# Performance work log

Hardware: AMD Instinct MI355X
Metric: run time of the kernel (lower is better)

Reference implementation:

```python
import jax, jax.numpy as jnp
import numpy as np
from jax import lax

EPS = 1e-5

def _ln(x, g, b):
    m = x.mean(-1, keepdims=True)
    v = x.var(-1, keepdims=True)
    return (x - m) * lax.rsqrt(v + EPS) * g + b

def _conv(x, w, b=None, groups=1, pad=0):
    y = lax.conv_general_dilated(x, w, (1, 1), [(pad, pad), (pad, pad)],
                                 feature_group_count=groups,
                                 dimension_numbers=('NCHW', 'OIHW', 'NCHW'))
    return y if b is None else y + b[None, :, None, None]

def _pscan(A, X):
    # linear recurrence h_t = A_t * h_{t-1} + X_t via associative scan over axis 1
    def comb(c1, c2):
        a1, x1 = c1
        a2, x2 = c2
        return a1 * a2, a2 * x1 + x2
    return lax.associative_scan(comb, (A, X), axis=1)[1]

def setup_inputs():
    B, T, D, H, W, K, E = 2, 24, 32, 64, 64, 3, 2
    key = jax.random.key(0)
    ks = jax.random.split(key, 30)
    r = lambda i, shp, s=1.0: jax.random.normal(ks[i], shp, jnp.float32) * s
    return dict(
        x_re=r(0, (B, T, D, H, W)), x_im=r(1, (B, T, D, H, W)),
        h_re=r(2, (B * H * W, 1, D)), h_im=r(3, (B * H * W, 1, D)),
        flux_re=r(4, (B, D), 0.5), flux_im=r(5, (B, D), 0.5),
        dt_seq=jax.random.uniform(ks[6], (B, T), jnp.float32, 0.05, 0.15),
        ln_s_g=jnp.ones((2 * D,)), ln_s_b=jnp.zeros((2 * D,)),
        conv_w=r(7, (2 * D, 2 * D, K, K), 0.05), conv_b=jnp.zeros((2 * D,)),
        ln_t_g=jnp.ones((2 * D,)), ln_t_b=jnp.zeros((2 * D,)),
        W_re=jnp.eye(D, dtype=jnp.float32) + r(8, (D, D), 0.1), W_im=r(9, (D, D), 0.1),
        lam_flux=r(10, (D,), 0.5), bf_re=r(11, (D,), 0.5), bf_im=r(12, (D,), 0.5),
        c_re=r(13, (D,), 0.5), c_im=r(14, (D,), 0.5),
        g_w=r(15, (D,), 0.5), g_b=jnp.zeros((D,)),
        a_decay=r(16, (D,), 0.5), b_freq=r(17, (D,), 0.5),
        ffn_w1=r(18, (2 * D, 2 * D * E), 0.05), ffn_b1=jnp.zeros((2 * D * E,)),
        ffn_w2=r(19, (2 * D * E, 2 * D), 0.05), ffn_b2=jnp.zeros((2 * D,)),
        sg_w1=r(20, (D, 2 * D, 1, 1), 0.05), sg_b1=jnp.zeros((D,)),
        sg_dw=r(21, (D, 1, 3, 3), 0.05),
        sg_w2=r(22, (D, D, 1, 1), 0.05), sg_b2=jnp.zeros((D,)),
    )

def reference(x_re, x_im, h_re, h_im, flux_re, flux_im, dt_seq,
              ln_s_g, ln_s_b, conv_w, conv_b, ln_t_g, ln_t_b,
              W_re, W_im, lam_flux, bf_re, bf_im, c_re, c_im, g_w, g_b,
              a_decay, b_freq, ffn_w1, ffn_b1, ffn_w2, ffn_b2,
              sg_w1, sg_b1, sg_dw, sg_w2, sg_b2):
    x = x_re + 1j * x_im                                  # [B,T,D,H,W] complex64
    B, T, D, H, W = x.shape
    K = conv_w.shape[-1]
    # ---- spatial (Clifford-style) conv with residual ----
    xf = x.reshape(B * T, D, H, W)
    xr = jnp.concatenate([xf.real, xf.imag], axis=1)      # [BT,2D,H,W]
    xn = _ln(xr.transpose(0, 2, 3, 1), ln_s_g, ln_s_b).transpose(0, 3, 1, 2)
    xs = _conv(xn, conv_w, conv_b, pad=K // 2)
    xf = xf + (xs[:, :D] + 1j * xs[:, D:])
    x = xf.reshape(B, T, D, H, W)
    # ---- eigen-basis encode ----
    Wb = W_re + 1j * W_im
    Wb_inv = jnp.linalg.inv(Wb)
    x_eig = jnp.einsum('bthwd,de->bthwe', x.transpose(0, 1, 3, 4, 2), Wb)  # [B,T,H,W,D]
    x_mean = x_eig.mean(axis=(2, 3))                      # [B,T,D]
    # ---- global flux scan over time ----
    dt = dt_seq[:, :, None]                               # [B,T,1]
    A_flux = jnp.exp(-jax.nn.softplus(lam_flux) * dt).astype(x_eig.dtype)  # [B,T,D]
    X_flux = (bf_re + 1j * bf_im) * x_mean * dt
    flux_seq = _pscan(A_flux, X_flux)
    flux_seq = flux_seq + (flux_re + 1j * flux_im)[:, None, :] * jnp.cumprod(A_flux, axis=1)
    source_seq = flux_seq * (c_re + 1j * c_im)            # [B,T,D] complex
    gate_seq = jax.nn.sigmoid(flux_seq.real * g_w + g_b)  # [B,T,D] real
    flux_out = flux_seq[:, -1]
    # ---- spatial gate modulation, batched over B*T (no python loop over T) ----
    xc = jnp.concatenate([x_eig.real, x_eig.imag], axis=-1)        # [B,T,H,W,2D]
    sf = xc.reshape(B * T, H, W, 2 * D).transpose(0, 3, 1, 2)
    g = jax.nn.silu(_conv(sf, sg_w1, sg_b1))
    g = _conv(g, sg_dw, None, groups=D, pad=1)
    g = jax.nn.sigmoid(_conv(g, sg_w2, sg_b2))                     # [BT,D,H,W]
    sp_gate = g.transpose(0, 2, 3, 1).reshape(B, T, H, W, D)
    gate_comb = gate_seq[:, :, None, None, :] * sp_gate            # [B,T,H,W,D]
    src = source_seq[:, :, None, None, :]
    forcing = x_eig * gate_comb + src * (1.0 - gate_comb)
    # ---- transition operators (ZOH discretization) ----
    lam = -jax.nn.softplus(a_decay) + 1j * b_freq                  # [D]
    op_decay = jnp.exp(lam * dt)                                   # [B,T,D] complex
    op_forcing = (op_decay - 1.0) / lam
    u_t = forcing * op_forcing[:, :, None, None, :]
    h_prev = (h_re + 1j * h_im).reshape(B, H, W, D)
    u_t = u_t.at[:, 0].add(h_prev * op_decay[:, 0][:, None, None, :])
    # ---- per-pixel temporal pscan ----
    A_full = jnp.broadcast_to(op_decay[:, :, None, None, :], u_t.shape)
    u_out = _pscan(A_full, u_t)                                    # [B,T,H,W,D]
    h_out = u_out[:, -1].reshape(B * H * W, 1, D)
    # ---- decode + temporal LN/FFN residual ----
    dec = jnp.einsum('bthwe,ed->bthwd', u_out, Wb_inv).transpose(0, 1, 4, 2, 3)
    df = dec.reshape(B * T, D, H, W)
    dr = jnp.concatenate([df.real, df.imag], axis=1).transpose(0, 2, 3, 1)  # [BT,H,W,2D]
    dn = _ln(dr, ln_t_g, ln_t_b)
    hid = jax.nn.silu(dn @ ffn_w1 + ffn_b1)
    out2 = hid @ ffn_w2 + ffn_b2
    delta = (out2[..., :D] + 1j * out2[..., D:]).transpose(0, 3, 1, 2)
    xo = (df + delta).reshape(B, T, D, H, W)
    z = x + xo
    out_main = jnp.stack([z.real, z.imag], axis=0)
    out_h = jnp.stack([h_out.real, h_out.imag], axis=0)
    out_flux = jnp.stack([flux_out.real, flux_out.imag], axis=0)
    return out_main, out_h, out_flux
```

## Files before the change

kernel.cpp:

```cpp
#include <hip/hip_runtime.h>
#include <math.h>

#define BB 2
#define TT 24
#define DD 32
#define HWp 4096
#define NN (BB*TT)
#define PIX (NN*HWp)
#define C2 (2*DD)

#define MAIN_RE 0
#define MAIN_IM (NN*DD*HWp)
#define HOUT_RE (2*NN*DD*HWp)
#define HOUT_IM (HOUT_RE + BB*HWp*DD)
#define FLUX_RE (HOUT_RE + 2*BB*HWp*DD)
#define FLUX_IM (FLUX_RE + BB*DD)

#define WS_XN   0
#define WS_XU   (WS_XN + PIX*32)
#define WS_XE   (WS_XU + PIX*32)
#define WS_G1   (WS_XE + PIX*C2)
#define WS_G2   (WS_G1 + PIX*DD)
#define WS_WINV (WS_G2 + PIX*DD)
#define WS_SUMS (WS_WINV + 2048)
#define WS_GATE (WS_SUMS + 3072)
#define WS_SRCR (WS_GATE + 1536)
#define WS_SRCI (WS_SRCR + 1536)
#define WS_ODR  (WS_SRCI + 1536)
#define WS_ODI  (WS_ODR + 1536)
#define WS_OFR  (WS_ODI + 1536)
#define WS_OFI  (WS_OFR + 1536)
#define WS_WPK  (WS_OFI + 1536)
#define WS_PART (WS_WPK + 18432)
#define WS_WE   (WS_PART + 49152)
#define WS_SG   (WS_WE + 2048)
#define WS_WIB  (WS_SG + 1024)

typedef __attribute__((ext_vector_type(8))) short bf16x8;
typedef __attribute__((ext_vector_type(4))) float f32x4;
union FU { unsigned u[4]; bf16x8 f; };
union FU4 { uint4 v; unsigned u[4]; bf16x8 f; };

__device__ __forceinline__ float sigmoidf_(float x) { return 1.f / (1.f + expf(-x)); }
__device__ __forceinline__ float softplusf_(float x) { return log1pf(expf(x)); }
__device__ __forceinline__ unsigned short f2bf(float f) {
  unsigned u = __float_as_uint(f);
  return (unsigned short)((u + 0x7FFFu + ((u >> 16) & 1u)) >> 16);
}
__device__ __forceinline__ unsigned pk2(float lo, float hi) {
  return (unsigned)f2bf(lo) | ((unsigned)f2bf(hi) << 16);
}
__device__ __forceinline__ float bf2f(unsigned short u) {
  return __uint_as_float((unsigned)u << 16);
}

__global__ void __launch_bounds__(256) k_prep(
    const float* __restrict__ xre, const float* __restrict__ xim,
    const float* __restrict__ g, const float* __restrict__ b,
    const float* __restrict__ Wre, const float* __restrict__ Wim,
    const float* __restrict__ conv_w, const float* __restrict__ sgw1,
    float* __restrict__ ws) {
  __shared__ float Mre[32][64];
  __shared__ float Mim[32][64];
  __shared__ float fre[32], fim[32];
  __shared__ int piv_s;
  int bid = blockIdx.x;
  int tid = threadIdx.x;

  if (bid < 768) {
    int gid = bid * 256 + tid;
    int n = gid >> 12, p = gid & 4095;
    float v[64];
    float s = 0.f;
#pragma unroll
    for (int c = 0; c < 32; ++c) { v[c] = xre[(n * 32 + c) * 4096 + p]; s += v[c]; }
#pragma unroll
    for (int c = 0; c < 32; ++c) { v[32 + c] = xim[(n * 32 + c) * 4096 + p]; s += v[32 + c]; }
    float m = s * (1.f / 64.f);
    float vs = 0.f;
#pragma unroll
    for (int c = 0; c < 64; ++c) { float d = v[c] - m; vs += d * d; }
    float rs = rsqrtf(vs * (1.f / 64.f) + 1e-5f);
#pragma unroll
    for (int c = 0; c < 64; ++c) v[c] = (v[c] - m) * rs * g[c] + b[c];
    uint4* dst = (uint4*)ws + gid * 8;
#pragma unroll
    for (int q = 0; q < 8; ++q) {
      uint4 u;
      u.x = pk2(v[q * 8 + 0], v[q * 8 + 1]);
      u.y = pk2(v[q * 8 + 2], v[q * 8 + 3]);
      u.z = pk2(v[q * 8 + 4], v[q * 8 + 5]);
      u.w = pk2(v[q * 8 + 6], v[q * 8 + 7]);
      dst[q] = u;
    }
    return;
  }

  if (bid == 768) {
    for (int idx = tid; idx < 2048; idx += 256) {
      int i = idx >> 6, j = idx & 63;
      if (j < 32) { Mre[i][j] = Wre[i * 32 + j]; Mim[i][j] = Wim[i * 32 + j]; }
      else        { Mre[i][j] = (j - 32 == i) ? 1.f : 0.f; Mim[i][j] = 0.f; }
    }
    __syncthreads();
    for (int k = 0; k < 32; ++k) {
      if (tid < 64) {
        int r = tid & 31;
        float mm = (r >= k) ? (fabsf(Mre[r][k]) + fabsf(Mim[r][k])) : -1.f;
        int best = r;
#pragma unroll
        for (int off = 16; off > 0; off >>= 1) {
          float m2 = __shfl_xor(mm, off);
          int b2 = __shfl_xor(best, off);
          if (m2 > mm || (m2 == mm && b2 < best)) { mm = m2; best = b2; }
        }
        if (tid == 0) piv_s = best;
      }
      __syncthreads();
      int pv = piv_s;
      if (pv != k && tid < 64) {
        float tr = Mre[k][tid], ti = Mim[k][tid];
        Mre[k][tid] = Mre[pv][tid]; Mim[k][tid] = Mim[pv][tid];
        Mre[pv][tid] = tr; Mim[pv][tid] = ti;
      }
      __syncthreads();
      float a = Mre[k][k], bq = Mim[k][k];
      float dd = a * a + bq * bq;
      float pr = a / dd, pi = -bq / dd;
      if (tid < 64) {
        float x = Mre[k][tid], y = Mim[k][tid];
        Mre[k][tid] = x * pr - y * pi;
        Mim[k][tid] = x * pi + y * pr;
      }
      __syncthreads();
      if (tid < 32) { fre[tid] = Mre[tid][k]; fim[tid] = Mim[tid][k]; }
      __syncthreads();
      for (int idx = tid; idx < 2048; idx += 256) {
        int i = idx >> 6, j = idx & 63;
        if (i != k) {
          float fr = fre[i], fi = fim[i];
          float ar = Mre[k][j], ai = Mim[k][j];
          Mre[i][j] -= fr * ar - fi * ai;
          Mim[i][j] -= fr * ai + fi * ar;
        }
      }
      __syncthreads();
    }
    unsigned* wib = (unsigned*)(ws + WS_WIB);
    for (int idx = tid; idx < 2048; idx += 256) {
      int j = idx >> 5, kp = idx & 31;
      float v[2];
#pragma unroll
      for (int h = 0; h < 2; ++h) {
        int k = 2 * kp + h;
        float x;
        if (j < 32) x = (k < 32) ? Mre[k][32 + j] : -Mim[k - 32][32 + j];
        else        x = (k < 32) ? Mim[k][32 + (j - 32)] : Mre[k - 32][32 + (j - 32)];
        v[h] = x;
      }
      wib[idx] = pk2(v[0], v[1]);
    }
    return;
  }

  if (bid <= 784) {
    int slice = bid - 769;
    unsigned short* wpk = (unsigned short*)(ws + WS_WPK);
#pragma unroll
    for (int i = 0; i < 9; ++i) {
      int idx = slice * 2304 + i * 256 + tid;
      int tap = idx >> 12;
      int rem = idx & 4095;
      int oc = rem >> 6, ci = rem & 63;
      wpk[idx] = f2bf(conv_w[(oc * 64 + ci) * 9 + tap]);
    }
    return;
  }

  {
    int t = (bid - 785) * 256 + tid;
    unsigned* we = (unsigned*)(ws + WS_WE);
    unsigned* sg = (unsigned*)(ws + WS_SG);
    {
      int oc = t >> 5, kp = t & 31;
      sg[t] = pk2(sgw1[oc * 64 + 2 * kp], sgw1[oc * 64 + 2 * kp + 1]);
    }
#pragma unroll
    for (int h2 = 0; h2 < 2; ++h2) {
      int idx = t + h2 * 1024;
      int j = idx >> 5, kp = idx & 31;
      float v[2];
#pragma unroll
      for (int h = 0; h < 2; ++h) {
        int k = 2 * kp + h;
        float x;
        if (j < 32) x = (k < 32) ? Wre[k * 32 + j] : -Wim[(k - 32) * 32 + j];
        else        x = (k < 32) ? Wim[k * 32 + (j - 32)] : Wre[(k - 32) * 32 + (j - 32)];
        v[h] = x;
      }
      we[idx] = pk2(v[0], v[1]);
    }
  }
}

__global__ void __launch_bounds__(256) k_conv(
    const unsigned* __restrict__ xnb_u, const unsigned short* __restrict__ wpk,
    const float* __restrict__ bconv,
    const float* __restrict__ xre, const float* __restrict__ xim,
    unsigned* __restrict__ xub) {
  __shared__ unsigned xls[6 * 66 * 36];
  int bid = blockIdx.x;
  int n = bid >> 4;
  int y0 = (bid & 15) * 4;
  int tid = threadIdx.x;
  int wv = tid >> 6, l = tid & 63;
  int l15 = l & 15, l4 = l >> 4;

  const uint4* xnb4 = (const uint4*)xnb_u;
  for (int idx = tid; idx < 396; idx += 256) {
    int r = idx / 66, c = idx - r * 66;
    int y = y0 - 1 + r, x = c - 1;
    bool valid = ((unsigned)y < 64u) & ((unsigned)x < 64u);
    int pg = n * 4096 + y * 64 + x;
    uint4 z; z.x = z.y = z.z = z.w = 0u;
#pragma unroll
    for (int q = 0; q < 8; ++q) {
      uint4 v = valid ? xnb4[pg * 8 + q] : z;
      *(uint4*)&xls[idx * 36 + q * 4] = v;
    }
  }
  __syncthreads();

  f32x4 acc[4][4];
#pragma unroll
  for (int Nt = 0; Nt < 4; ++Nt) {
    float bb = bconv[Nt * 16 + l15];
#pragma unroll
    for (int mt = 0; mt < 4; ++mt) acc[mt][Nt] = (f32x4){bb, bb, bb, bb};
  }

  const uint4* wq = (const uint4*)wpk;
#pragma unroll
  for (int tap = 0; tap < 9; ++tap) {
    int ky = tap / 3, kx = tap - ky * 3;
    int rowbase = (wv + ky) * 66 + kx + l15;
#pragma unroll
    for (int ks = 0; ks < 2; ++ks) {
      FU4 B[4];
#pragma unroll
      for (int Nt = 0; Nt < 4; ++Nt)
        B[Nt].v = wq[tap * 512 + (Nt * 16 + l15) * 8 + ks * 4 + l4];
#pragma unroll
      for (int mt = 0; mt < 4; ++mt) {
        FU4 A;
        A.v = *(const uint4*)&xls[(rowbase + mt * 16) * 36 + ks * 16 + l4 * 4];
#pragma unroll
        for (int Nt = 0; Nt < 4; ++Nt)
          acc[mt][Nt] = __builtin_amdgcn_mfma_f32_16x16x32_bf16(A.f, B[Nt].f, acc[mt][Nt], 0, 0, 0);
      }
    }
  }
  __syncthreads();

  unsigned short (*xsb)[66] = (unsigned short(*)[66])xls;
#pragma unroll
  for (int Nt = 0; Nt < 4; ++Nt) {
    int oc = Nt * 16 + l15;
    int d = oc & 31;
    const float* resid = (oc < 32) ? xre : xim;
    const float* rsd = resid + (n * 32 + d) * 4096;
#pragma unroll
    for (int mt = 0; mt < 4; ++mt) {
      int lp0 = wv * 64 + mt * 16 + l4 * 4;
      int pixbase = y0 * 64 + lp0;
#pragma unroll
      for (int r = 0; r < 4; ++r)
        xsb[lp0 + r][oc] = f2bf(rsd[pixbase + r] + acc[mt][Nt][r]);
    }
  }
  __syncthreads();

  int pixG0 = n * 4096 + y0 * 64;
#pragma unroll
  for (int i = 0; i < 8; ++i) {
    int idx = tid + 256 * i;
    int lp = idx >> 3, q4 = idx & 7;
    uint4 v;
    v.x = xls[lp * 33 + q4 * 4 + 0];
    v.y = xls[lp * 33 + q4 * 4 + 1];
    v.z = xls[lp * 33 + q4 * 4 + 2];
    v.w = xls[lp * 33 + q4 * 4 + 3];
    ((uint4*)xub)[(pixG0 + lp) * 8 + q4] = v;
  }
}

__global__ void __launch_bounds__(256) k_xeig(
    const unsigned* __restrict__ xub, const unsigned* __restrict__ weP,
    const unsigned* __restrict__ sgP, unsigned short* __restrict__ xeb,
    float* __restrict__ g1, const float* __restrict__ sgb1,
    float* __restrict__ part) {
  __shared__ unsigned WeT[64][35];
  __shared__ unsigned SgT[32][35];
  __shared__ unsigned xp[64][35];
  __shared__ float xef[64][67];

  int tid = threadIdx.x;
  int gbase = blockIdx.x * 256;
  int l = tid & 63, wv = tid >> 6;
  int l15 = l & 15, l4 = l >> 4;
  int p64 = l, q = wv;
  const uint4* xub4 = (const uint4*)xub;

  {
#pragma unroll
    for (int i = 0; i < 8; ++i) {
      int idx = tid + i * 256;
      WeT[idx >> 5][idx & 31] = weP[idx];
    }
#pragma unroll
    for (int i = 0; i < 4; ++i) {
      int idx = tid + i * 256;
      SgT[idx >> 5][idx & 31] = sgP[idx];
    }
  }
  float ssum[16];
#pragma unroll
  for (int i = 0; i < 16; ++i) ssum[i] = 0.f;
  __syncthreads();

  for (int ph = 0; ph < 4; ++ph) {
    int gg = gbase + ph * 64 + p64;
    int arow = wv * 16 + l15;
    int pixG = gbase + ph * 64 + arow;

    FU4 a0, a1;
    a0.v = xub4[pixG * 8 + l4];
    a1.v = xub4[pixG * 8 + 4 + l4];
#pragma unroll
    for (int Nt = 0; Nt < 4; ++Nt) {
      f32x4 acc = (f32x4){0.f, 0.f, 0.f, 0.f};
      FU b0f, b1f;
      int brow = Nt * 16 + l15;
#pragma unroll
      for (int jj = 0; jj < 4; ++jj) {
        b0f.u[jj] = WeT[brow][l4 * 4 + jj];
        b1f.u[jj] = WeT[brow][16 + l4 * 4 + jj];
      }
      acc = __builtin_amdgcn_mfma_f32_16x16x32_bf16(a0.f, b0f.f, acc, 0, 0, 0);
      acc = __builtin_amdgcn_mfma_f32_16x16x32_bf16(a1.f, b1f.f, acc, 0, 0, 0);
#pragma unroll
      for (int r = 0; r < 4; ++r)
        xef[wv * 16 + l4 * 4 + r][Nt * 16 + l15] = acc[r];
    }
    __syncthreads();

    float xo[16];
#pragma unroll
    for (int i = 0; i < 16; ++i) {
      xo[i] = xef[p64][q * 16 + i];
      ssum[i] += xo[i];
      xeb[(q * 16 + i) * PIX + gg] = f2bf(xo[i]);
    }
#pragma unroll
    for (int ii = 0; ii < 8; ++ii)
      xp[p64][q * 8 + ii] = pk2(xo[2 * ii], xo[2 * ii + 1]);
    __syncthreads();

    FU c0, c1;
#pragma unroll
    for (int jj = 0; jj < 4; ++jj) {
      c0.u[jj] = xp[arow][l4 * 4 + jj];
      c1.u[jj] = xp[arow][16 + l4 * 4 + jj];
    }
#pragma unroll
    for (int Nt = 0; Nt < 2; ++Nt) {
      float bb = sgb1[Nt * 16 + l15];
      f32x4 acc = (f32x4){bb, bb, bb, bb};
      FU b0f, b1f;
      int brow = Nt * 16 + l15;
#pragma unroll
      for (int jj = 0; jj < 4; ++jj) {
        b0f.u[jj] = SgT[brow][l4 * 4 + jj];
        b1f.u[jj] = SgT[brow][16 + l4 * 4 + jj];
      }
      acc = __builtin_amdgcn_mfma_f32_16x16x32_bf16(c0.f, b0f.f, acc, 0, 0, 0);
      acc = __builtin_amdgcn_mfma_f32_16x16x32_bf16(c1.f, b1f.f, acc, 0, 0, 0);
#pragma unroll
      for (int r = 0; r < 4; ++r) {
        float v = acc[r];
        xef[wv * 16 + l4 * 4 + r][Nt * 16 + l15] = v * sigmoidf_(v);
      }
    }
    __syncthreads();

#pragma unroll
    for (int i = 0; i < 8; ++i)
      g1[(q * 8 + i) * PIX + gg] = xef[p64][q * 8 + i];
    __syncthreads();
  }

#pragma unroll
  for (int i = 0; i < 16; ++i) {
    float v = ssum[i];
    v += __shfl_xor(v, 1);
    v += __shfl_xor(v, 2);
    v += __shfl_xor(v, 4);
    v += __shfl_xor(v, 8);
    v += __shfl_xor(v, 16);
    v += __shfl_xor(v, 32);
    if (l == 0) part[blockIdx.x * 64 + q * 16 + i] = v;
  }
}

__global__ void k_flux(float* __restrict__ ws, float* __restrict__ out,
                       const float* __restrict__ dt_seq,
                       const float* __restrict__ flux_re, const float* __restrict__ flux_im,
                       const float* __restrict__ lam_flux,
                       const float* __restrict__ bf_re, const float* __restrict__ bf_im,
                       const float* __restrict__ c_re, const float* __restrict__ c_im,
                       const float* __restrict__ g_w, const float* __restrict__ g_b,
                       const float* __restrict__ a_decay, const float* __restrict__ b_freq) {
  int tid = threadIdx.x;
  if (tid >= 64) return;
  int b = tid >> 5, e = tid & 31;
  float sp_lf = softplusf_(lam_flux[e]);
  float lr = -softplusf_(a_decay[e]);
  float li = b_freq[e];
  float den = lr * lr + li * li;
  float bfr = bf_re[e], bfi = bf_im[e];
  float cr = c_re[e], ci = c_im[e];
  float fr = flux_re[b * 32 + e], fi = flux_im[b * 32 + e];
  const float* part = ws + WS_PART;
  for (int t = 0; t < 24; ++t) {
    int n = b * 24 + t;
    float dt = dt_seq[n];
    float A = expf(-sp_lf * dt);
    float xmr = 0.f, xmi = 0.f;
#pragma unroll
    for (int j = 0; j < 16; ++j) {
      xmr += part[(n * 16 + j) * 64 + e];
      xmi += part[(n * 16 + j) * 64 + 32 + e];
    }
    xmr *= (1.f / 4096.f);
    xmi *= (1.f / 4096.f);
    float Xr = (bfr * xmr - bfi * xmi) * dt;
    float Xi = (bfr * xmi + bfi * xmr) * dt;
    fr = A * fr + Xr;
    fi = A * fi + Xi;
    ws[WS_GATE + n * 32 + e] = sigmoidf_(fr * g_w[e] + g_b[e]);
    ws[WS_SRCR + n * 32 + e] = fr * cr - fi * ci;
    ws[WS_SRCI + n * 32 + e] = fr * ci + fi * cr;
    float er = expf(lr * dt);
    float odr = er * cosf(li * dt);
    float odi = er * sinf(li * dt);
    ws[WS_ODR + n * 32 + e] = odr;
    ws[WS_ODI + n * 32 + e] = odi;
    float nr = odr - 1.f, ni = odi;
    ws[WS_OFR + n * 32 + e] = (nr * lr + ni * li) / den;
    ws[WS_OFI + n * 32 + e] = (ni * lr - nr * li) / den;
  }
  out[FLUX_RE + b * 32 + e] = fr;
  out[FLUX_IM + b * 32 + e] = fi;
}

__global__ void __launch_bounds__(256) k_gate(
    const float* __restrict__ g1, float* __restrict__ spgP,
    const float* __restrict__ dw, const float* __restrict__ w2,
    const float* __restrict__ b2) {
  __shared__ float g2s[128][33];
  int tid = threadIdx.x;
  int l = tid & 63;
  int wv = tid >> 6;
  int r = wv >> 1, h = wv & 1;
  int pixbase = blockIdx.x * 128;
  int n = pixbase >> 12;
  int y = ((pixbase & 4095) >> 6) + r;
  int g = pixbase + r * 64 + l;
  int rp = r * 64 + l;

#pragma unroll
  for (int c = 0; c < 16; ++c) {
    int oc = h * 16 + c;
    const float* src = g1 + oc * PIX + n * 4096;
    const float* w = dw + oc * 9;
    float r0 = (y > 0)  ? src[(y - 1) * 64 + l] : 0.f;
    float r1 = src[y * 64 + l];
    float r2 = (y < 63) ? src[(y + 1) * 64 + l] : 0.f;
    float l0 = __shfl_up(r0, 1), t0 = __shfl_down(r0, 1);
    float l1 = __shfl_up(r1, 1), t1 = __shfl_down(r1, 1);
    float l2 = __shfl_up(r2, 1), t2 = __shfl_down(r2, 1);
    if (l == 0)  { l0 = 0.f; l1 = 0.f; l2 = 0.f; }
    if (l == 63) { t0 = 0.f; t1 = 0.f; t2 = 0.f; }
    float acc = 0.f;
    acc = fmaf(l0, w[0], acc); acc = fmaf(r0, w[1], acc); acc = fmaf(t0, w[2], acc);
    acc = fmaf(l1, w[3], acc); acc = fmaf(r1, w[4], acc); acc = fmaf(t1, w[5], acc);
    acc = fmaf(l2, w[6], acc); acc = fmaf(r2, w[7], acc); acc = fmaf(t2, w[8], acc);
    g2s[rp][oc] = acc;
  }
  __syncthreads();
  float g2a[32];
#pragma unroll
  for (int c = 0; c < 32; ++c) g2a[c] = g2s[rp][c];

#pragma unroll
  for (int c = 0; c < 16; ++c) {
    int e = h * 16 + c;
    float acc = b2[e];
#pragma unroll
    for (int k = 0; k < 32; ++k)
      acc = fmaf(g2a[k], w2[e * 32 + k], acc);
    spgP[e * PIX + g] = sigmoidf_(acc);
  }
}

__global__ void __launch_bounds__(256) k_scan(
    unsigned short* __restrict__ ub, const float* __restrict__ spgP,
    const float* __restrict__ gate, const float* __restrict__ srcr,
    const float* __restrict__ srci, const float* __restrict__ ofr_p,
    const float* __restrict__ ofi_p, const float* __restrict__ odr_p,
    const float* __restrict__ odi_p,
    const float* __restrict__ hre, const float* __restrict__ him,
    float* __restrict__ out) {
  int p = blockIdx.x * 256 + threadIdx.x;
  int e = blockIdx.y;
  int b = blockIdx.z;
  float ur = 0.f, ui = 0.f;
  for (int t = 0; t < 24; ++t) {
    int n = b * 24 + t;
    int ie = n * 32 + e;
    int idx  = e * PIX + n * 4096 + p;
    int idxi = (32 + e) * PIX + n * 4096 + p;
    float gc = gate[ie] * spgP[idx];
    float xr = bf2f(ub[idx]), xi = bf2f(ub[idxi]);
    float om = 1.f - gc;
    float fr2 = xr * gc + srcr[ie] * om;
    float fi2 = xi * gc + srci[ie] * om;
    float ofr = ofr_p[ie], ofi = ofi_p[ie];
    float utr = fr2 * ofr - fi2 * ofi;
    float uti = fr2 * ofi + fi2 * ofr;
    if (t == 0) {
      int hb = (b * 4096 + p) * 32 + e;
      float hr = hre[hb], hi = him[hb];
      float odr0 = odr_p[ie], odi0 = odi_p[ie];
      utr += hr * odr0 - hi * odi0;
      uti += hr * odi0 + hi * odr0;
    }
    float ar = odr_p[ie], ai = odi_p[ie];
    float nr = ar * ur - ai * ui + utr;
    float ni = ar * ui + ai * ur + uti;
    ur = nr; ui = ni;
    ub[idx] = f2bf(ur);
    ub[idxi] = f2bf(ui);
  }
  out[HOUT_RE + (b * 4096 + p) * 32 + e] = ur;
  out[HOUT_IM + (b * 4096 + p) * 32 + e] = ui;
}

__global__ void __launch_bounds__(256) k_final(
    const unsigned short* __restrict__ ub, const unsigned* __restrict__ xub,
    float* __restrict__ out, const unsigned* __restrict__ wibP,
    const float* __restrict__ lg, const float* __restrict__ lb,
    const float* __restrict__ w1, const float* __restrict__ b1,
    const float* __restrict__ w2, const float* __restrict__ b2) {
  __shared__ unsigned wiT[64][35];
  __shared__ unsigned w1T[128][35];
  __shared__ unsigned w2T[64][67];
  __shared__ unsigned dnp[64][35];
  __shared__ unsigned ho[64][67];
  __shared__ float ps1[64][5];
  __shared__ float ps2[64][5];

  int tid = threadIdx.x;
  int gbase = blockIdx.x * 256;
  int l = tid & 63, wv = tid >> 6;
  int l15 = l & 15, l4 = l >> 4;
  int p64 = l, q = wv;
  const uint4* xub4 = (const uint4*)xub;

  {
#pragma unroll
    for (int i = 0; i < 8; ++i) {
      int idx = tid + i * 256;
      wiT[idx >> 5][idx & 31] = wibP[idx];
    }
    int hid = tid & 127, half = tid >> 7;
#pragma unroll
    for (int i = 0; i < 16; ++i) {
      int cp = half * 16 + i;
      w1T[hid][cp] = pk2(w1[(2 * cp) * 128 + hid], w1[(2 * cp + 1) * 128 + hid]);
    }
#pragma unroll
    for (int i = 0; i < 16; ++i) {
      int hp = wv * 16 + i;
      w2T[l][hp] = pk2(w2[(2 * hp) * 64 + l], w2[(2 * hp + 1) * 64 + l]);
    }
  }
  float bb1v[8], bb2v[4];
#pragma unroll
  for (int Hn = 0; Hn < 8; ++Hn) bb1v[Hn] = b1[Hn * 16 + l15];
#pragma unroll
  for (int On = 0; On < 4; ++On) bb2v[On] = b2[On * 16 + l15];

  unsigned uvp[8];
  FU4 xa, xb;
  {
    int gg = gbase + p64;
#pragma unroll
    for (int ii = 0; ii < 8; ++ii) {
      int c0 = q * 16 + 2 * ii;
      unsigned lo = ub[c0 * PIX + gg];
      unsigned hi = ub[(c0 + 1) * PIX + gg];
      uvp[ii] = lo | (hi << 16);
    }
    xa.v = xub4[gg * 8 + q * 2];
    xb.v = xub4[gg * 8 + q * 2 + 1];
  }
  __syncthreads();

  for (int ph = 0; ph < 4; ++ph) {
    int gg = gbase + ph * 64 + p64;
    int arow = wv * 16 + l15;

#pragma unroll
    for (int ii = 0; ii < 8; ++ii)
      dnp[p64][q * 8 + ii] = uvp[ii];
    if (ph < 3) {
      int gg2 = gg + 64;
#pragma unroll
      for (int ii = 0; ii < 8; ++ii) {
        int c0 = q * 16 + 2 * ii;
        unsigned lo = ub[c0 * PIX + gg2];
        unsigned hi = ub[(c0 + 1) * PIX + gg2];
        uvp[ii] = lo | (hi << 16);
      }
    }
    __syncthreads();

    {
      FU a0, a1;
#pragma unroll
      for (int jj = 0; jj < 4; ++jj) {
        a0.u[jj] = dnp[arow][l4 * 4 + jj];
        a1.u[jj] = dnp[arow][16 + l4 * 4 + jj];
      }
      float (*decf)[67] = (float(*)[67])ho;
#pragma unroll
      for (int Nt = 0; Nt < 4; ++Nt) {
        f32x4 acc = (f32x4){0.f, 0.f, 0.f, 0.f};
        FU b0f, b1f;
        int brow = Nt * 16 + l15;
#pragma unroll
        for (int jj = 0; jj < 4; ++jj) {
          b0f.u[jj] = wiT[brow][l4 * 4 + jj];
          b1f.u[jj] = wiT[brow][16 + l4 * 4 + jj];
        }
        acc = __builtin_amdgcn_mfma_f32_16x16x32_bf16(a0.f, b0f.f, acc, 0, 0, 0);
        acc = __builtin_amdgcn_mfma_f32_16x16x32_bf16(a1.f, b1f.f, acc, 0, 0, 0);
#pragma unroll
        for (int r = 0; r < 4; ++r)
          decf[wv * 16 + l4 * 4 + r][Nt * 16 + l15] = acc[r];
      }
    }
    __syncthreads();

    float dv[16];
    float s1 = 0.f, s2 = 0.f;
    {
      float (*decf)[67] = (float(*)[67])ho;
#pragma unroll
      for (int i = 0; i < 16; ++i) {
        dv[i] = decf[p64][q * 16 + i];
        s1 += dv[i];
        s2 += dv[i] * dv[i];
      }
    }
    ps1[p64][q] = s1;
    ps2[p64][q] = s2;
    __syncthreads();
    float m  = (ps1[p64][0] + ps1[p64][1] + ps1[p64][2] + ps1[p64][3]) * (1.f / 64.f);
    float e2 = (ps2[p64][0] + ps2[p64][1] + ps2[p64][2] + ps2[p64][3]) * (1.f / 64.f);
    float rs = rsqrtf(e2 - m * m + 1e-5f);
#pragma unroll
    for (int ii = 0; ii < 8; ++ii) {
      int c0 = q * 16 + 2 * ii;
      float a = (dv[2 * ii]     - m) * rs * lg[c0]     + lb[c0];
      float bvl = (dv[2 * ii + 1] - m) * rs * lg[c0 + 1] + lb[c0 + 1];
      dnp[p64][q * 8 + ii] = pk2(a, bvl);
    }
    __syncthreads();

    FU a0, a1;
#pragma unroll
    for (int jj = 0; jj < 4; ++jj) {
      a0.u[jj] = dnp[arow][l4 * 4 + jj];
      a1.u[jj] = dnp[arow][16 + l4 * 4 + jj];
    }
    f32x4 acc[8];
#pragma unroll
    for (int Hn = 0; Hn < 8; ++Hn) {
      float bb = bb1v[Hn];
      acc[Hn] = (f32x4){bb, bb, bb, bb};
      FU b0f, b1f;
      int brow = Hn * 16 + l15;
#pragma unroll
      for (int jj = 0; jj < 4; ++jj) {
        b0f.u[jj] = w1T[brow][l4 * 4 + jj];
        b1f.u[jj] = w1T[brow][16 + l4 * 4 + jj];
      }
      acc[Hn] = __builtin_amdgcn_mfma_f32_16x16x32_bf16(a0.f, b0f.f, acc[Hn], 0, 0, 0);
      acc[Hn] = __builtin_amdgcn_mfma_f32_16x16x32_bf16(a1.f, b1f.f, acc[Hn], 0, 0, 0);
    }
    unsigned short (*hidb)[134] = (unsigned short(*)[134])ho;
#pragma unroll
    for (int Hn = 0; Hn < 8; ++Hn) {
#pragma unroll
      for (int r = 0; r < 4; ++r) {
        float v = acc[Hn][r];
        v = v * sigmoidf_(v);
        hidb[wv * 16 + l4 * 4 + r][Hn * 16 + l15] = f2bf(v);
      }
    }
    __syncthreads();

    FU a2[4];
#pragma unroll
    for (int kk = 0; kk < 4; ++kk)
#pragma unroll
      for (int jj = 0; jj < 4; ++jj)
        a2[kk].u[jj] = ((unsigned(*)[67])ho)[arow][kk * 16 + l4 * 4 + jj];
    f32x4 acc2[4];
#pragma unroll
    for (int On = 0; On < 4; ++On) {
      float bb = bb2v[On];
      acc2[On] = (f32x4){bb, bb, bb, bb};
#pragma unroll
      for (int kk = 0; kk < 4; ++kk) {
        FU b2f;
#pragma unroll
        for (int jj = 0; jj < 4; ++jj)
          b2f.u[jj] = w2T[On * 16 + l15][kk * 16 + l4 * 4 + jj];
        acc2[On] = __builtin_amdgcn_mfma_f32_16x16x32_bf16(a2[kk].f, b2f.f, acc2[On], 0, 0, 0);
      }
    }
    float (*o2f)[67] = (float(*)[67])ho;
#pragma unroll
    for (int On = 0; On < 4; ++On)
#pragma unroll
      for (int r = 0; r < 4; ++r)
        o2f[wv * 16 + l4 * 4 + r][On * 16 + l15] = acc2[On][r];
    __syncthreads();

    {
      int nn = gg >> 12, pim = gg & 4095;
#pragma unroll
      for (int ii = 0; ii < 8; ++ii) {
        unsigned w = (ii < 4) ? xa.u[ii] : xb.u[ii - 4];
        float x0 = __uint_as_float(w << 16);
        float x1 = __uint_as_float(w & 0xFFFF0000u);
        int c0 = q * 16 + 2 * ii;
#pragma unroll
        for (int h = 0; h < 2; ++h) {
          int c = c0 + h;
          float xv = (h == 0) ? x0 : x1;
          float val = xv + o2f[p64][c] + dv[2 * ii + h];
          int d = c & 31;
          long off = ((c < 32) ? (long)MAIN_RE : (long)MAIN_IM) + (long)(nn * 32 + d) * 4096 + pim;
          out[off] = val;
        }
      }
      if (ph < 3) {
        int gg2 = gg + 64;
        xa.v = xub4[gg2 * 8 + q * 2];
        xb.v = xub4[gg2 * 8 + q * 2 + 1];
      }
    }
    __syncthreads();
  }
}

extern "C" void kernel_launch(void* const* d_in, const int* in_sizes, int n_in,
                              void* d_out, int out_size, void* d_ws, size_t ws_size,
                              hipStream_t stream) {
  (void)in_sizes; (void)n_in; (void)out_size; (void)ws_size;
  const float* xre      = (const float*)d_in[0];
  const float* xim      = (const float*)d_in[1];
  const float* hre      = (const float*)d_in[2];
  const float* him      = (const float*)d_in[3];
  const float* flux_re  = (const float*)d_in[4];
  const float* flux_im  = (const float*)d_in[5];
  const float* dt_seq   = (const float*)d_in[6];
  const float* ln_s_g   = (const float*)d_in[7];
  const float* ln_s_b   = (const float*)d_in[8];
  const float* conv_w   = (const float*)d_in[9];
  const float* conv_b   = (const float*)d_in[10];
  const float* ln_t_g   = (const float*)d_in[11];
  const float* ln_t_b   = (const float*)d_in[12];
  const float* W_re     = (const float*)d_in[13];
  const float* W_im     = (const float*)d_in[14];
  const float* lam_flux = (const float*)d_in[15];
  const float* bf_re    = (const float*)d_in[16];
  const float* bf_im    = (const float*)d_in[17];
  const float* c_re     = (const float*)d_in[18];
  const float* c_im     = (const float*)d_in[19];
  const float* g_w      = (const float*)d_in[20];
  const float* g_b      = (const float*)d_in[21];
  const float* a_decay  = (const float*)d_in[22];
  const float* b_freq   = (const float*)d_in[23];
  const float* ffn_w1   = (const float*)d_in[24];
  const float* ffn_b1   = (const float*)d_in[25];
  const float* ffn_w2   = (const float*)d_in[26];
  const float* ffn_b2   = (const float*)d_in[27];
  const float* sg_w1    = (const float*)d_in[28];
  const float* sg_b1    = (const float*)d_in[29];
  const float* sg_dw    = (const float*)d_in[30];
  const float* sg_w2    = (const float*)d_in[31];
  const float* sg_b2    = (const float*)d_in[32];
  float* out = (float*)d_out;
  float* ws  = (float*)d_ws;

  unsigned* xub = (unsigned*)(ws + WS_XU);
  unsigned short* xeb = (unsigned short*)(ws + WS_XE);

  k_prep<<<789, 256, 0, stream>>>(xre, xim, ln_s_g, ln_s_b, W_re, W_im,
                                  conv_w, sg_w1, ws);
  k_conv<<<768, 256, 0, stream>>>((const unsigned*)(ws + WS_XN),
                                  (const unsigned short*)(ws + WS_WPK),
                                  conv_b, xre, xim, xub);
  k_xeig<<<768, 256, 0, stream>>>(xub, (const unsigned*)(ws + WS_WE),
                                  (const unsigned*)(ws + WS_SG),
                                  xeb, ws + WS_G1, sg_b1, ws + WS_PART);
  k_flux<<<1, 64, 0, stream>>>(ws, out, dt_seq, flux_re, flux_im, lam_flux,
                               bf_re, bf_im, c_re, c_im, g_w, g_b, a_decay, b_freq);
  k_gate<<<PIX / 128, 256, 0, stream>>>(ws + WS_G1, ws + WS_G2, sg_dw, sg_w2, sg_b2);
  k_scan<<<dim3(4096 / 256, 32, 2), 256, 0, stream>>>(xeb, ws + WS_G2,
                                                      ws + WS_GATE, ws + WS_SRCR, ws + WS_SRCI,
                                                      ws + WS_OFR, ws + WS_OFI,
                                                      ws + WS_ODR, ws + WS_ODI,
                                                      hre, him, out);
  k_final<<<768, 256, 0, stream>>>(xeb, xub, out, (const unsigned*)(ws + WS_WIB),
                                   ln_t_g, ln_t_b, ffn_w1, ffn_b1, ffn_w2, ffn_b2);
}
```

Measured before the change: 293.2 us.

## Move complex matrix inversion from prep kernel into conv kernel block zero

The serial 32-step Gauss-Jordan inversion of the complex eigenbasis matrix was one block of k_prep and could set that kernel's tail latency. It now runs as an extra block 0 of k_conv, reusing that kernel's shared-memory tile, so it overlaps with the convolution blocks. The pivot step is also tightened: pivot search, reciprocal and row swap/scale are merged to remove two barriers per iteration. The risk is that the long inversion block now sets k_conv's tail instead, and shared-memory reuse has to stay correct.

After: 238.9 us. 1.23x faster.

```diff
diff --git a/kernel.cpp b/kernel.cpp
--- a/kernel.cpp
+++ b/kernel.cpp
@@ -60,10 +60,6 @@
     const float* __restrict__ Wre, const float* __restrict__ Wim,
     const float* __restrict__ conv_w, const float* __restrict__ sgw1,
     float* __restrict__ ws) {
-  __shared__ float Mre[32][64];
-  __shared__ float Mim[32][64];
-  __shared__ float fre[32], fim[32];
-  __shared__ int piv_s;
   int bid = blockIdx.x;
   int tid = threadIdx.x;
 
@@ -96,75 +92,8 @@
     return;
   }
 
-  if (bid == 768) {
-    for (int idx = tid; idx < 2048; idx += 256) {
-      int i = idx >> 6, j = idx & 63;
-      if (j < 32) { Mre[i][j] = Wre[i * 32 + j]; Mim[i][j] = Wim[i * 32 + j]; }
-      else        { Mre[i][j] = (j - 32 == i) ? 1.f : 0.f; Mim[i][j] = 0.f; }
-    }
-    __syncthreads();
-    for (int k = 0; k < 32; ++k) {
-      if (tid < 64) {
-        int r = tid & 31;
-        float mm = (r >= k) ? (fabsf(Mre[r][k]) + fabsf(Mim[r][k])) : -1.f;
-        int best = r;
-#pragma unroll
-        for (int off = 16; off > 0; off >>= 1) {
-          float m2 = __shfl_xor(mm, off);
-          int b2 = __shfl_xor(best, off);
-          if (m2 > mm || (m2 == mm && b2 < best)) { mm = m2; best = b2; }
-        }
-        if (tid == 0) piv_s = best;
-      }
-      __syncthreads();
-      int pv = piv_s;
-      if (pv != k && tid < 64) {
-        float tr = Mre[k][tid], ti = Mim[k][tid];
-        Mre[k][tid] = Mre[pv][tid]; Mim[k][tid] = Mim[pv][tid];
-        Mre[pv][tid] = tr; Mim[pv][tid] = ti;
-      }
-      __syncthreads();
-      float a = Mre[k][k], bq = Mim[k][k];
-      float dd = a * a + bq * bq;
-      float pr = a / dd, pi = -bq / dd;
-      if (tid < 64) {
-        float x = Mre[k][tid], y = Mim[k][tid];
-        Mre[k][tid] = x * pr - y * pi;
-        Mim[k][tid] = x * pi + y * pr;
-      }
-      __syncthreads();
-      if (tid < 32) { fre[tid] = Mre[tid][k]; fim[tid] = Mim[tid][k]; }
-      __syncthreads();
-      for (int idx = tid; idx < 2048; idx += 256) {
-        int i = idx >> 6, j = idx & 63;
-        if (i != k) {
-          float fr = fre[i], fi = fim[i];
-          float ar = Mre[k][j], ai = Mim[k][j];
-          Mre[i][j] -= fr * ar - fi * ai;
-          Mim[i][j] -= fr * ai + fi * ar;
-        }
-      }
-      __syncthreads();
-    }
-    unsigned* wib = (unsigned*)(ws + WS_WIB);
-    for (int idx = tid; idx < 2048; idx += 256) {
-      int j = idx >> 5, kp = idx & 31;
-      float v[2];
-#pragma unroll
-      for (int h = 0; h < 2; ++h) {
-        int k = 2 * kp + h;
-        float x;
-        if (j < 32) x = (k < 32) ? Mre[k][32 + j] : -Mim[k - 32][32 + j];
-        else        x = (k < 32) ? Mim[k][32 + (j - 32)] : Mre[k - 32][32 + (j - 32)];
-        v[h] = x;
-      }
-      wib[idx] = pk2(v[0], v[1]);
-    }
-    return;
-  }
-
-  if (bid <= 784) {
-    int slice = bid - 769;
+  if (bid <= 783) {
+    int slice = bid - 768;
     unsigned short* wpk = (unsigned short*)(ws + WS_WPK);
 #pragma unroll
     for (int i = 0; i < 9; ++i) {
@@ -178,7 +107,7 @@
   }
 
   {
-    int t = (bid - 785) * 256 + tid;
+    int t = (bid - 784) * 256 + tid;
     unsigned* we = (unsigned*)(ws + WS_WE);
     unsigned* sg = (unsigned*)(ws + WS_SG);
     {
@@ -207,12 +136,94 @@
     const unsigned* __restrict__ xnb_u, const unsigned short* __restrict__ wpk,
     const float* __restrict__ bconv,
     const float* __restrict__ xre, const float* __restrict__ xim,
-    unsigned* __restrict__ xub) {
+    unsigned* __restrict__ xub,
+    const float* __restrict__ Wre, const float* __restrict__ Wim,
+    unsigned* __restrict__ wib) {
   __shared__ unsigned xls[6 * 66 * 36];
+  __shared__ int piv_s;
+  __shared__ float prs[2];
   int bid = blockIdx.x;
-  int n = bid >> 4;
-  int y0 = (bid & 15) * 4;
   int tid = threadIdx.x;
+
+  if (bid == 0) {
+    float* Mre = (float*)xls;
+    float* Mim = (float*)xls + 2048;
+    float* fre = (float*)xls + 4096;
+    float* fim = (float*)xls + 4128;
+    for (int idx = tid; idx < 2048; idx += 256) {
+      int i = idx >> 6, j = idx & 63;
+      if (j < 32) { Mre[idx] = Wre[i * 32 + j]; Mim[idx] = Wim[i * 32 + j]; }
+      else        { Mre[idx] = (j - 32 == i) ? 1.f : 0.f; Mim[idx] = 0.f; }
+    }
+    __syncthreads();
+    for (int k = 0; k < 32; ++k) {
+      if (tid < 32) {
+        int r = tid;
+        float re = Mre[r * 64 + k], im = Mim[r * 64 + k];
+        float mm = (r >= k) ? (fabsf(re) + fabsf(im)) : -1.f;
+        int best = r;
+#pragma unroll
+        for (int off = 16; off > 0; off >>= 1) {
+          float m2 = __shfl_xor(mm, off);
+          int b2 = __shfl_xor(best, off);
+          if (m2 > mm || (m2 == mm && b2 < best)) { mm = m2; best = b2; }
+        }
+        float pvr = __shfl(re, best);
+        float pvi = __shfl(im, best);
+        if (tid == 0) {
+          float dd = pvr * pvr + pvi * pvi;
+          piv_s = best;
+          prs[0] = pvr / dd;
+          prs[1] = -pvi / dd;
+        }
+      }
+      __syncthreads();
+      int pv = piv_s;
+      float pr = prs[0], pi = prs[1];
+      if (tid < 64) {
+        int l = tid;
+        float kr = Mre[k * 64 + l], ki = Mim[k * 64 + l];
+        float vr = Mre[pv * 64 + l], vi = Mim[pv * 64 + l];
+        Mre[pv * 64 + l] = kr; Mim[pv * 64 + l] = ki;
+        Mre[k * 64 + l] = vr * pr - vi * pi;
+        Mim[k * 64 + l] = vr * pi + vi * pr;
+        if (l == k) { fre[pv] = kr; fim[pv] = ki; }
+        if (l < 32 && l != pv && l != k) {
+          fre[l] = Mre[l * 64 + k];
+          fim[l] = Mim[l * 64 + k];
+        }
+      }
+      __syncthreads();
+      for (int idx = tid; idx < 2048; idx += 256) {
+        int i = idx >> 6, j = idx & 63;
+        if (i != k) {
+          float fr = fre[i], fi2 = fim[i];
+          float ar = Mre[k * 64 + j], ai = Mim[k * 64 + j];
+          Mre[idx] -= fr * ar - fi2 * ai;
+          Mim[idx] -= fr * ai + fi2 * ar;
+        }
+      }
+      __syncthreads();
+    }
+    for (int idx = tid; idx < 2048; idx += 256) {
+      int j = idx >> 5, kp = idx & 31;
+      float v[2];
+#pragma unroll
+      for (int h = 0; h < 2; ++h) {
+        int kk = 2 * kp + h;
+        float x;
+        if (j < 32) x = (kk < 32) ? Mre[kk * 64 + 32 + j] : -Mim[(kk - 32) * 64 + 32 + j];
+        else        x = (kk < 32) ? Mim[kk * 64 + 32 + (j - 32)] : Mre[(kk - 32) * 64 + 32 + (j - 32)];
+        v[h] = x;
+      }
+      wib[idx] = pk2(v[0], v[1]);
+    }
+    return;
+  }
+
+  int cb = bid - 1;
+  int n = cb >> 4;
+  int y0 = (cb & 15) * 4;
   int wv = tid >> 6, l = tid & 63;
   int l15 = l & 15, l4 = l >> 4;
 
@@ -821,11 +832,12 @@
   unsigned* xub = (unsigned*)(ws + WS_XU);
   unsigned short* xeb = (unsigned short*)(ws + WS_XE);
 
-  k_prep<<<789, 256, 0, stream>>>(xre, xim, ln_s_g, ln_s_b, W_re, W_im,
+  k_prep<<<788, 256, 0, stream>>>(xre, xim, ln_s_g, ln_s_b, W_re, W_im,
                                   conv_w, sg_w1, ws);
-  k_conv<<<768, 256, 0, stream>>>((const unsigned*)(ws + WS_XN),
+  k_conv<<<769, 256, 0, stream>>>((const unsigned*)(ws + WS_XN),
                                   (const unsigned short*)(ws + WS_WPK),
-                                  conv_b, xre, xim, xub);
+                                  conv_b, xre, xim, xub,
+                                  W_re, W_im, (unsigned*)(ws + WS_WIB));
   k_xeig<<<768, 256, 0, stream>>>(xub, (const unsigned*)(ws + WS_WE),
                                   (const unsigned*)(ws + WS_SG),
                                   xeb, ws + WS_G1, sg_b1, ws + WS_PART);
```
